# Performance work log

Hardware: AMD Instinct MI355X
Metric: run time of the kernel (lower is better)

## Reference

```python
import jax, jax.numpy as jnp
import numpy as np

B, C, S, H, W = 1, 256, 64, 32, 128
BLOCKS, HEADS, DH = 2, 8, 32
SCALE = DH ** (-0.5)


def layer_norm(x, w, b, eps=1e-5):
    mu = jnp.mean(x, axis=-1, keepdims=True)
    var = jnp.var(x, axis=-1, keepdims=True)
    return (x - mu) * jax.lax.rsqrt(var + eps) * w + b


def generate_y_for_attn(y, u):
    # y: (B,C,H,W), u: (B,S,S) float -> (B, S^2, 2H, C)
    Bv, Cv, Hv, Wv = y.shape
    Sv = u.shape[1]
    uf = jnp.floor(u).reshape(Bv, Sv * Sv)
    u_left = jnp.clip(uf, 0, Wv - 1).astype(jnp.int32)
    u_right = jnp.clip(uf + 1, 0, Wv - 1).astype(jnp.int32)
    yf = y.reshape(Bv, Cv * Hv, Wv)

    def gather_w(idx):
        idxb = jnp.broadcast_to(idx[:, None, :], (Bv, Cv * Hv, Sv * Sv))
        return jnp.take_along_axis(yf, idxb, axis=2).reshape(Bv, Cv, Hv, Sv * Sv)

    ys = jnp.concatenate([gather_w(u_left), gather_w(u_right)], axis=2)  # (B,C,2H,S2)
    return ys.transpose(0, 3, 2, 1)  # (B, S2, 2H, C)


def cross_attention(x, y, p, i):
    # x: (B,M,C), y: (B,M,N,C)
    q = layer_norm(x, p['ln_q_w'][i], p['ln_q_b'][i]) @ p['Wq'][i]        # (B,M,HD)
    k = layer_norm(y, p['ln_k_w'][i], p['ln_k_b'][i]) @ p['Wk'][i]        # (B,M,N,HD)
    v = layer_norm(y, p['ln_v_w'][i], p['ln_v_b'][i]) @ p['Wv'][i]        # (B,M,N,HD)
    Bv, M, _ = q.shape
    N = k.shape[2]
    q = q.reshape(Bv, M, HEADS, DH)
    k = k.reshape(Bv, M, N, HEADS, DH)
    v = v.reshape(Bv, M, N, HEADS, DH)
    dot = SCALE * jnp.einsum('bmhd,bmnhd->bhmn', q, k)                    # (B,H,M,N)
    attn = jax.nn.softmax(dot, axis=-1)
    a = jnp.einsum('bhmn,bmnhd->bmhd', attn, v).reshape(Bv, M, HEADS * DH)
    z = a @ p['Wproj'][i] + p['bproj'][i]
    z = layer_norm(z, p['ln_pre_w'][i], p['ln_pre_b'][i])
    h = jax.nn.gelu(z @ p['Wm1'][i] + p['bm1'][i], approximate=False)
    z = z + (h @ p['Wm2'][i] + p['bm2'][i])
    return layer_norm(z, p['ln_post_w'][i], p['ln_post_b'][i])


def setup_inputs() -> dict:
    key = jax.random.key(0)
    ks = jax.random.split(key, 16)
    std = 0.02
    inp = {
        'grd2sat': jax.random.normal(ks[0], (B, C, S, S), jnp.float32),
        'grd_x': jax.random.normal(ks[1], (B, C, H, W), jnp.float32),
        'u': jax.random.uniform(ks[2], (B, S, S), jnp.float32) * (W - 1),
        'ln_q_w': jnp.ones((BLOCKS, C)), 'ln_q_b': jnp.zeros((BLOCKS, C)),
        'ln_k_w': jnp.ones((BLOCKS, C)), 'ln_k_b': jnp.zeros((BLOCKS, C)),
        'ln_v_w': jnp.ones((BLOCKS, C)), 'ln_v_b': jnp.zeros((BLOCKS, C)),
        'Wq': std * jax.random.normal(ks[3], (BLOCKS, C, HEADS * DH)),
        'Wk': std * jax.random.normal(ks[4], (BLOCKS, C, HEADS * DH)),
        'Wv': std * jax.random.normal(ks[5], (BLOCKS, C, HEADS * DH)),
        'Wproj': std * jax.random.normal(ks[6], (BLOCKS, HEADS * DH, C)),
        'bproj': jnp.zeros((BLOCKS, C)),
        'ln_pre_w': jnp.ones((BLOCKS, C)), 'ln_pre_b': jnp.zeros((BLOCKS, C)),
        'Wm1': std * jax.random.normal(ks[7], (BLOCKS, C, 2 * C)),
        'bm1': jnp.zeros((BLOCKS, 2 * C)),
        'Wm2': std * jax.random.normal(ks[8], (BLOCKS, 2 * C, C)),
        'bm2': jnp.zeros((BLOCKS, C)),
        'ln_post_w': jnp.ones((BLOCKS, C)), 'ln_post_b': jnp.zeros((BLOCKS, C)),
    }
    return inp


def reference(grd2sat, grd_x, u, ln_q_w, ln_q_b, ln_k_w, ln_k_b, ln_v_w, ln_v_b,
              Wq, Wk, Wv, Wproj, bproj, ln_pre_w, ln_pre_b, Wm1, bm1, Wm2, bm2,
              ln_post_w, ln_post_b):
    p = dict(ln_q_w=ln_q_w, ln_q_b=ln_q_b, ln_k_w=ln_k_w, ln_k_b=ln_k_b,
             ln_v_w=ln_v_w, ln_v_b=ln_v_b, Wq=Wq, Wk=Wk, Wv=Wv, Wproj=Wproj,
             bproj=bproj, ln_pre_w=ln_pre_w, ln_pre_b=ln_pre_b, Wm1=Wm1, bm1=bm1,
             Wm2=Wm2, bm2=bm2, ln_post_w=ln_post_w, ln_post_b=ln_post_b)
    y_attn = generate_y_for_attn(grd_x, u)               # (B, S^2, 2H, C)
    x = grd2sat.reshape(B, C, S * S).transpose(0, 2, 1)  # (B, M, C)
    for i in range(BLOCKS):
        # (Swin self-attention layer omitted; cross-attention stack only.)
        x = cross_attention(x, y_attn, p, i)
    out = x.transpose(0, 2, 1).reshape(B, C, S, S)
    # L2 normalize over channel dim
    norm = jnp.sqrt(jnp.sum(out * out, axis=1, keepdims=True))
    return out / jnp.maximum(norm, 1e-12)
```

## Files before the change

### kernel.cpp

```cpp
#include <hip/hip_runtime.h>
#include <math.h>


#define C_DIM 256
#define M_DIM 4096
#define W_DIM 128
#define H_DIM 32
#define ATT_SCALE 0.17677669529663687f

typedef __attribute__((ext_vector_type(8))) short short8;
typedef __attribute__((ext_vector_type(4))) short short4v;
typedef __attribute__((ext_vector_type(4))) float floatx4;

__device__ __forceinline__ unsigned short f2bf(float f) {
    unsigned u = __float_as_uint(f);
    unsigned r = (u + 0x7fffu + ((u >> 16) & 1u)) >> 16;
    return (unsigned short)r;
}
__device__ __forceinline__ float gelu_exact(float x) {
    return 0.5f * x * (1.0f + erff(x * 0.70710678118654752f));
}

struct PrepArgs {
    const float* grd2sat; float* xcur;
// ... 92 lines not shown
        o.z = f2bf(tile[rq + 2][cl]);
        o.w = f2bf(tile[rq + 3][cl]);
        *(ushort4*)&out[(size_t)(c0 + cl) * R + r0 + rq] = o;
    } else if (b < 1418) {
        int jj = b - 1408;
        int N = a.fN[jj];
        int wcol = a.fwcol[jj] + t;
        const float* W = a.fW[jj];
        const float* lb = a.flnb[jj];
        float s = a.fbase[jj] ? a.fbase[jj][wcol] : 0.f;
        for (int k = 0; k < 256; ++k) s += lb[k] * W[(size_t)k * N + wcol];
        a.fout[jj][a.focol[jj] + t] = s;
    } else {
        int* hist = (int*)smemf;
        int* cur = (int*)smemf + 128;
        unsigned short* wlb = (unsigned short*)((int*)smemf + 256);
        if (t < 128) hist[t] = 0;
        __syncthreads();
        for (int it = 0; it < 16; ++it) {
            int m = it * 256 + t;
            int wl = (int)floorf(a.u[m]);
            wl = max(0, min(wl, 126));
            wlb[m] = (unsigned short)wl;
            atomicAdd(&hist[wl], 1);
        }
        __syncthreads();
        if (t == 0) {
            int run = 0, nc = 0;
            for (int bkt = 0; bkt < 127; ++bkt) {
                int c = hist[bkt];
                cur[bkt] = run;
                int q0 = run;
                while (c > 0) {
                    int take = min(c, 32);
                    a.chunks[nc] = make_int4(bkt, q0, take, 0);
                    ++nc; q0 += take; c -= take;
                }
                run += hist[bkt];
            }
            *a.nchunks = nc;
        }
        __syncthreads();
        for (int it = 0; it < 16; ++it) {
            int m = it * 256 + t;
            int wl = wlb[m];
            int pos = atomicAdd(&cur[wl], 1);
            a.perm[pos] = m;
        }
    }
}

struct GJ {
    const float* A; const unsigned short* Bt;
    const float* bias; const float* aw; const float* ab;
    const float* rw; const float* rb; const float* res;
    float* wrz; void* out; unsigned short* out2;
    int K, N;
};

template <int LN, int EPI, int OUTM, bool WRZ>
__device__ __forceinline__ void gemm_core(const GJ& j, short (*As)[264],
                                          short (*Bs)[264], int bm, int by) {
    int t = threadIdx.x;
    int bn = by << 6;
    int wv = t >> 6, lane = t & 63;
    int mt = wv & 1, nt0 = (wv >> 1) << 1;
    int quad = lane >> 4, l16 = lane & 15;
    floatx4 acc0 = {0.f, 0.f, 0.f, 0.f};
    floatx4 acc1 = {0.f, 0.f, 0.f, 0.f};
    const int K = j.K;
    for (int kc = 0; kc < K; kc += 256) {
        if (kc) __syncthreads();
        {
            int ar = t >> 3, cq = (t & 7) << 2;
            const float* ap = j.A + (size_t)(bm + ar) * K + kc + cq;
            float4 v[8];
#pragma unroll
            for (int g = 0; g < 8; ++g) v[g] = *(const float4*)(ap + g * 32);
            if (LN >= 1) {
                float s = 0.f, ss = 0.f;
#pragma unroll
                for (int g = 0; g < 8; ++g) {
                    s += v[g].x + v[g].y + v[g].z + v[g].w;
                    ss += v[g].x * v[g].x + v[g].y * v[g].y + v[g].z * v[g].z +
                          v[g].w * v[g].w;
                }
#pragma unroll
                for (int o = 1; o < 8; o <<= 1) {
                    s += __shfl_xor(s, o, 64);
                    ss += __shfl_xor(ss, o, 64);
                }
                float mu = s * (1.f / 256.f);
                float rs = rsqrtf(ss * (1.f / 256.f) - mu * mu + 1e-5f);
#pragma unroll
                for (int g = 0; g < 8; ++g) {
                    v[g].x = (v[g].x - mu) * rs;
                    v[g].y = (v[g].y - mu) * rs;
                    v[g].z = (v[g].z - mu) * rs;
                    v[g].w = (v[g].w - mu) * rs;
                }
                if (LN == 2) {
                    float s2 = 0.f, ss2 = 0.f;
#pragma unroll
                    for (int g = 0; g < 8; ++g) {
                        float4 w4 = *(const float4*)(j.aw + cq + g * 32);
                        float4 b4 = *(const float4*)(j.ab + cq + g * 32);
                        v[g].x = v[g].x * w4.x + b4.x;
                        v[g].y = v[g].y * w4.y + b4.y;
                        v[g].z = v[g].z * w4.z + b4.z;
                        v[g].w = v[g].w * w4.w + b4.w;
                        s2 += v[g].x + v[g].y + v[g].z + v[g].w;
                        ss2 += v[g].x * v[g].x + v[g].y * v[g].y +
                               v[g].z * v[g].z + v[g].w * v[g].w;
                    }
#pragma unroll
                    for (int o = 1; o < 8; o <<= 1) {
                        s2 += __shfl_xor(s2, o, 64);
                        ss2 += __shfl_xor(ss2, o, 64);
                    }
                    float mu2 = s2 * (1.f / 256.f);
                    float rs2 = rsqrtf(ss2 * (1.f / 256.f) - mu2 * mu2 + 1e-5f);
#pragma unroll
                    for (int g = 0; g < 8; ++g) {
                        v[g].x = (v[g].x - mu2) * rs2;
                        v[g].y = (v[g].y - mu2) * rs2;
                        v[g].z = (v[g].z - mu2) * rs2;
                        v[g].w = (v[g].w - mu2) * rs2;
                    }
                }
            }
            if (WRZ) {
                if (by == 0) {
#pragma unroll
                    for (int g = 0; g < 8; ++g)
                        *(float4*)&j.wrz[(size_t)(bm + ar) * 256 + cq + g * 32] =
                            v[g];
                }
            }
#pragma unroll
            for (int g = 0; g < 8; ++g) {
                short4v o;
                o[0] = (short)f2bf(v[g].x);
                o[1] = (short)f2bf(v[g].y);
                o[2] = (short)f2bf(v[g].z);
                o[3] = (short)f2bf(v[g].w);
                *(short4v*)&As[ar][cq + g * 32] = o;
            }
        }
        {
            int br = t >> 2, cq2 = (t & 3) << 3;
            const unsigned short* bp = j.Bt + (size_t)(bn + br) * K + kc + cq2;
#pragma unroll
            for (int g = 0; g < 8; ++g)
                *(short8*)&Bs[br][cq2 + g * 32] = *(const short8*)(bp + g * 32);
        }
        __syncthreads();
#pragma unroll
        for (int k0 = 0; k0 < 8; ++k0) {
            short8 aa = *(const short8*)&As[(mt << 4) + l16][(k0 << 5) + (quad << 3)];
            short8 b0 = *(const short8*)&Bs[(nt0 << 4) + l16][(k0 << 5) + (quad << 3)];
            short8 b1 =
                *(const short8*)&Bs[((nt0 + 1) << 4) + l16][(k0 << 5) + (quad << 3)];
            acc0 = __builtin_amdgcn_mfma_f32_16x16x32_bf16(aa, b0, acc0, 0, 0, 0);
            acc1 = __builtin_amdgcn_mfma_f32_16x16x32_bf16(aa, b1, acc1, 0, 0, 0);
        }
    }
#pragma unroll
    for (int jj = 0; jj < 2; ++jj) {
        const floatx4 accv = jj ? acc1 : acc0;
        int col = bn + ((nt0 + jj) << 4) + l16;
        float bv = j.bias ? j.bias[col] : 0.f;
#pragma unroll
        for (int r = 0; r < 4; ++r) {
            int row = bm + (mt << 4) + (quad << 2) + r;
            float v = accv[r] + bv;
            if (EPI == 1) v = gelu_exact(v);
            if (EPI == 2)
                v += j.res[(size_t)row * 256 + col] * j.rw[col] + j.rb[col];
            if (OUTM == 0) {
                ((float*)j.out)[(size_t)row * j.N + col] = v;
            } else if (OUTM == 1) {
                ((unsigned short*)j.out)[(size_t)row * 256 + col] = f2bf(v);
            } else {
                if (col < 256)
                    ((unsigned short*)j.out)[(size_t)row * 256 + col] = f2bf(v);
                else
                    j.out2[(size_t)(col - 256) * M_DIM + row] = f2bf(v);
            }
        }
    }
}

template <int MODE>
__global__ __launch_bounds__(256) void gemm_mode(GJ j0, GJ j1) {
    __shared__ short As[32][264];
    __shared__ short Bs[64][264];
    int bm = blockIdx.x << 5;
    if (MODE == 0) {
        if ((int)blockIdx.y < 4) gemm_core<1, 0, 1, false>(j0, As, Bs, bm, blockIdx.y);
        else gemm_core<0, 0, 2, false>(j1, As, Bs, bm, blockIdx.y - 4);
    } else if (MODE == 1) {
        if ((int)blockIdx.y < 4) gemm_core<2, 0, 1, false>(j0, As, Bs, bm, blockIdx.y);
        else gemm_core<0, 0, 2, false>(j1, As, Bs, bm, blockIdx.y - 4);
    } else if (MODE == 2) {
        gemm_core<0, 0, 0, false>(j0, As, Bs, bm, blockIdx.y);
    } else if (MODE == 3) {
        gemm_core<1, 1, 0, true>(j0, As, Bs, bm, blockIdx.y);
    } else {
        gemm_core<0, 2, 0, false>(j0, As, Bs, bm, blockIdx.y);
    }
}

__global__ __launch_bounds__(256) void attn_kernel(
    const unsigned short* __restrict__ Qb, const unsigned short* __restrict__ Kt,
    const unsigned short* __restrict__ Vt, const int* __restrict__ perm,
    const int4* __restrict__ chunks, const int* __restrict__ nchunks,
    float* __restrict__ Ao) {
    __shared__ short Qs[32][264];
    __shared__ short Ks[64][264];
    __shared__ short VsT[256][72];
    __shared__ float S[32][69];
    __shared__ short Pb[32][72];
    __shared__ int gperm[32];
    if ((int)blockIdx.x >= *nchunks) return;
    int4 cd = chunks[blockIdx.x];
    int wl = cd.x, qstart = cd.y, qcnt = cd.z;
    int t = threadIdx.x;
    if (t < 32) gperm[t] = (t < qcnt) ? perm[qstart + t] : 0;
    {
        int q = t >> 3, p = t & 7;
        if (q < qcnt) {
            const uint4* src =
                (const uint4*)(Qb + (size_t)perm[qstart + q] * 256 + (p << 5));
#pragma unroll
            for (int c = 0; c < 4; ++c) *(uint4*)&Qs[q][(p << 5) + (c << 3)] = src[c];
        } else {
            uint4 z = make_uint4(0, 0, 0, 0);
#pragma unroll
            for (int c = 0; c < 4; ++c) *(uint4*)&Qs[q][(p << 5) + (c << 3)] = z;
        }
    }
    {
        int n = t >> 2, p = t & 3;
        const uint4* src = (const uint4*)(Kt + ((size_t)(wl * 32 + n)) * 256 + (p << 6));
#pragma unroll
        for (int c = 0; c < 8; ++c) *(uint4*)&Ks[n][(p << 6) + (c << 3)] = src[c];
    }
    {
        const uint4* src = (const uint4*)(Vt + (size_t)t * M_DIM + (wl << 5));
#pragma unroll
        for (int c = 0; c < 8; ++c) *(uint4*)&VsT[t][c << 3] = src[c];
    }
    __syncthreads();
    int wv = t >> 6, lane = t & 63, quad = lane >> 4, l16 = lane & 15;
    int mtS = wv & 1, ntS0 = (wv >> 1) << 1;
    int mtP = wv & 1, ntP = wv >> 1;
    int sq = t >> 3, sg = t & 7;
#pragma unroll 1
    for (int h = 0; h < 8; ++h) {
        {
            short8 aa = *(const short8*)&Qs[(mtS << 4) + l16][(h << 5) + (quad << 3)];
            short8 b0 = *(const short8*)&Ks[(ntS0 << 4) + l16][(h << 5) + (quad << 3)];
            short8 b1 =
                *(const short8*)&Ks[((ntS0 + 1) << 4) + l16][(h << 5) + (quad << 3)];
            floatx4 z = {0.f, 0.f, 0.f, 0.f};
            floatx4 c0 = __builtin_amdgcn_mfma_f32_16x16x32_bf16(aa, b0, z, 0, 0, 0);
            floatx4 c1 = __builtin_amdgcn_mfma_f32_16x16x32_bf16(aa, b1, z, 0, 0, 0);
#pragma unroll
            for (int r = 0; r < 4; ++r) {
                int row = (mtS << 4) + (quad << 2) + r;
                S[row][(ntS0 << 4) + l16] = c0[r];
                S[row][((ntS0 + 1) << 4) + l16] = c1[r];
            }
        }
        __syncthreads();
        {
            float e[8];
            float s = 0.f;
#pragma unroll
            for (int c = 0; c < 8; ++c) {
                e[c] = __expf(S[sq][(sg << 3) + c] * ATT_SCALE);
                s += e[c];
            }
            s += __shfl_xor(s, 1, 64);
            s += __shfl_xor(s, 2, 64);
            s += __shfl_xor(s, 4, 64);
            float ri = 1.f / s;
#pragma unroll
            for (int c = 0; c < 8; ++c)
                Pb[sq][(sg << 3) + c] = (short)f2bf(e[c] * ri);
        }
        __syncthreads();
        {
            floatx4 acc = {0.f, 0.f, 0.f, 0.f};
#pragma unroll
            for (int ks = 0; ks < 2; ++ks) {
                short8 aa =
                    *(const short8*)&Pb[(mtP << 4) + l16][(ks << 5) + (quad << 3)];
                short8 bb = *(const short8*)&VsT[(h << 5) + (ntP << 4) + l16]
                                                [(ks << 5) + (quad << 3)];
                acc = __builtin_amdgcn_mfma_f32_16x16x32_bf16(aa, bb, acc, 0, 0, 0);
            }
#pragma unroll
            for (int r = 0; r < 4; ++r) {
                int q = (mtP << 4) + (quad << 2) + r;
                if (q < qcnt)
                    Ao[(size_t)gperm[q] * C_DIM + (h << 5) + (ntP << 4) + l16] =
                        acc[r];
            }
        }
        __syncthreads();
    }
}

__global__ __launch_bounds__(256) void out_kernel(const float* __restrict__ X,
                                                  const float* __restrict__ w,
                                                  const float* __restrict__ b,
                                                  float* __restrict__ out) {
    __shared__ float tile[64][65];
    int t = threadIdx.x;
    int mo = t >> 2, q = t & 3;
    int m0 = blockIdx.x << 6;
    const float* p = X + (size_t)(m0 + mo) * C_DIM + (q << 6);
    float4 v[16];
    float s = 0.f, ss = 0.f;
#pragma unroll
    for (int c = 0; c < 16; ++c) {
        v[c] = *(const float4*)(p + c * 4);
        s += v[c].x + v[c].y + v[c].z + v[c].w;
        ss += v[c].x * v[c].x + v[c].y * v[c].y + v[c].z * v[c].z + v[c].w * v[c].w;
    }
    s += __shfl_xor(s, 1, 64); s += __shfl_xor(s, 2, 64);
    ss += __shfl_xor(ss, 1, 64); ss += __shfl_xor(ss, 2, 64);
    float mu = s * (1.f / 256.f);
    float rs = rsqrtf(ss * (1.f / 256.f) - mu * mu + 1e-5f);
    float ss2 = 0.f;
#pragma unroll
    for (int c = 0; c < 16; ++c) {
        float4 w4 = *(const float4*)&w[(q << 6) + c * 4];
        float4 b4 = *(const float4*)&b[(q << 6) + c * 4];
        v[c].x = (v[c].x - mu) * rs * w4.x + b4.x;
        v[c].y = (v[c].y - mu) * rs * w4.y + b4.y;
        v[c].z = (v[c].z - mu) * rs * w4.z + b4.z;
        v[c].w = (v[c].w - mu) * rs * w4.w + b4.w;
// ... 20 lines not shown
        __syncthreads();
    }
}

extern "C" void kernel_launch(void* const* d_in, const int* in_sizes, int n_in,
                              void* d_out, int out_size, void* d_ws, size_t ws_size,
                              hipStream_t stream) {
    const float* grd2sat = (const float*)d_in[0];
    const float* grd_x   = (const float*)d_in[1];
    const float* u       = (const float*)d_in[2];
    const float* ln_q_w  = (const float*)d_in[3];
    const float* ln_q_b  = (const float*)d_in[4];
    const float* ln_k_w  = (const float*)d_in[5];
    const float* ln_k_b  = (const float*)d_in[6];
    const float* ln_v_w  = (const float*)d_in[7];
    const float* ln_v_b  = (const float*)d_in[8];
    const float* Wq      = (const float*)d_in[9];
    const float* Wk      = (const float*)d_in[10];
    const float* Wv      = (const float*)d_in[11];
    const float* Wproj   = (const float*)d_in[12];
    const float* bproj   = (const float*)d_in[13];
    const float* ln_pre_w = (const float*)d_in[14];
    const float* ln_pre_b = (const float*)d_in[15];
    const float* Wm1     = (const float*)d_in[16];
    const float* bm1     = (const float*)d_in[17];
    const float* Wm2     = (const float*)d_in[18];
    const float* bm2     = (const float*)d_in[19];
    const float* ln_post_w = (const float*)d_in[20];
    const float* ln_post_b = (const float*)d_in[21];

    float* ws   = (float*)d_ws;
    float* yhat = ws;
    float* xcur = ws + 1048576;
    float* zq   = ws + 2097152;
    float* abuf = ws + 3145728;
    float* hbuf = ws + 4194304;
    float* zbuf = ws + 6291456;
    unsigned short* Qb   = (unsigned short*)(ws + 7340032);
    unsigned short* Ktab = (unsigned short*)(ws + 7864320);
    unsigned short* Vt   = (unsigned short*)(ws + 8388608);
    unsigned short* Bt   = (unsigned short*)(ws + 8912896);
    float* biasbuf = ws + 9961472;
    int*  perm    = (int*)(ws + 9965568);
    int4* chunks  = (int4*)(ws + 9969664);
    int*  nchunks = (int*)(ws + 9970688);
    const size_t BS = 524288;
    const size_t OQ = 0, OKV = 65536, OP = 196608, OM1 = 262144, OM2 = 393216;

    dim3 b256(256);

    PrepArgs pa;
    pa.grd2sat = grd2sat; pa.xcur = xcur;
    pa.grd_x = grd_x;     pa.yhat = yhat;
    pa.u = u; pa.perm = perm; pa.chunks = chunks; pa.nchunks = nchunks;
    {
        int base = 0;
        for (int i = 0; i < 2; ++i) {
            int e = 6 * i;
            unsigned short* bt = Bt + i * BS;
            pa.win[e+0] = Wq + i * 65536;    pa.wout[e+0] = bt + OQ;
            pa.wlnw[e+0] = ln_q_w + i * 256; pa.wR[e+0] = 256; pa.wC[e+0] = 256;
            pa.win[e+1] = Wk + i * 65536;    pa.wout[e+1] = bt + OKV;
            pa.wlnw[e+1] = ln_k_w + i * 256; pa.wR[e+1] = 256; pa.wC[e+1] = 256;
            pa.win[e+2] = Wv + i * 65536;    pa.wout[e+2] = bt + OKV + 65536;
            pa.wlnw[e+2] = ln_v_w + i * 256; pa.wR[e+2] = 256; pa.wC[e+2] = 256;
            pa.win[e+3] = Wproj + i * 65536; pa.wout[e+3] = bt + OP;
            pa.wlnw[e+3] = nullptr;          pa.wR[e+3] = 256; pa.wC[e+3] = 256;
            pa.win[e+4] = Wm1 + i * 131072;  pa.wout[e+4] = bt + OM1;
            pa.wlnw[e+4] = ln_pre_w + i * 256; pa.wR[e+4] = 256; pa.wC[e+4] = 512;
            pa.win[e+5] = Wm2 + i * 131072;  pa.wout[e+5] = bt + OM2;
            pa.wlnw[e+5] = nullptr;          pa.wR[e+5] = 512; pa.wC[e+5] = 256;
        }
        for (int e = 0; e < 12; ++e) {
            pa.wbase[e] = base;
            base += (pa.wR[e] >> 5) * (pa.wC[e] >> 5);
        }
        pa.wbase[12] = base;
        for (int i = 0; i < 2; ++i) {
            int jb = 5 * i;
            float* bb = biasbuf + i * 1280;
            pa.fW[jb+0] = Wq + i * 65536; pa.flnb[jb+0] = ln_q_b + i * 256;
            pa.fbase[jb+0] = nullptr; pa.fout[jb+0] = bb;
            pa.fN[jb+0] = 256; pa.fwcol[jb+0] = 0; pa.focol[jb+0] = 0;
            pa.fW[jb+1] = Wk + i * 65536; pa.flnb[jb+1] = ln_k_b + i * 256;
            pa.fbase[jb+1] = nullptr; pa.fout[jb+1] = bb + 256;
            pa.fN[jb+1] = 256; pa.fwcol[jb+1] = 0; pa.focol[jb+1] = 0;
            pa.fW[jb+2] = Wv + i * 65536; pa.flnb[jb+2] = ln_v_b + i * 256;
            pa.fbase[jb+2] = nullptr; pa.fout[jb+2] = bb + 256;
            pa.fN[jb+2] = 256; pa.fwcol[jb+2] = 0; pa.focol[jb+2] = 256;
            pa.fW[jb+3] = Wm1 + i * 131072; pa.flnb[jb+3] = ln_pre_b + i * 256;
            pa.fbase[jb+3] = bm1 + i * 512; pa.fout[jb+3] = bb + 768;
            pa.fN[jb+3] = 512; pa.fwcol[jb+3] = 0; pa.focol[jb+3] = 0;
            pa.fW[jb+4] = Wm1 + i * 131072; pa.flnb[jb+4] = ln_pre_b + i * 256;
            pa.fbase[jb+4] = bm1 + i * 512; pa.fout[jb+4] = bb + 768;
            pa.fN[jb+4] = 512; pa.fwcol[jb+4] = 256; pa.focol[jb+4] = 256;
        }
    }
    prep_kernel<<<1419, b256, 0, stream>>>(pa);

    for (int i = 0; i < 2; ++i) {
        const unsigned short* bt = Bt + i * BS;
        float* bb = biasbuf + i * 1280;
        GJ jq = {};
        jq.A = xcur; jq.Bt = bt + OQ; jq.bias = bb;
        if (i == 1) { jq.aw = ln_post_w; jq.ab = ln_post_b; }
        jq.out = Qb; jq.K = 256; jq.N = 256;
        GJ jkv = {};
        jkv.A = yhat; jkv.Bt = bt + OKV; jkv.bias = bb + 256;
        jkv.out = Ktab; jkv.out2 = Vt; jkv.K = 256; jkv.N = 512;
        if (i == 0) gemm_mode<0><<<dim3(128, 12), b256, 0, stream>>>(jq, jkv);
        else        gemm_mode<1><<<dim3(128, 12), b256, 0, stream>>>(jq, jkv);

        attn_kernel<<<255, b256, 0, stream>>>(Qb, Ktab, Vt, perm, chunks,
                                              nchunks, abuf);

        GJ jp = {};
        jp.A = abuf; jp.Bt = bt + OP; jp.bias = bproj + i * 256;
        jp.out = zq; jp.K = 256; jp.N = 256;
        gemm_mode<2><<<dim3(128, 4), b256, 0, stream>>>(jp, jp);

        GJ jm1 = {};
        jm1.A = zq; jm1.Bt = bt + OM1; jm1.bias = bb + 768;
        jm1.out = hbuf; jm1.wrz = zbuf; jm1.K = 256; jm1.N = 512;
        gemm_mode<3><<<dim3(128, 8), b256, 0, stream>>>(jm1, jm1);

        GJ jm2 = {};
        jm2.A = hbuf; jm2.Bt = bt + OM2; jm2.bias = bm2 + i * 256;
        jm2.res = zbuf; jm2.rw = ln_pre_w + i * 256; jm2.rb = ln_pre_b + i * 256;
        jm2.out = xcur; jm2.K = 512; jm2.N = 256;
        gemm_mode<4><<<dim3(128, 4), b256, 0, stream>>>(jm2, jm2);
    }
    out_kernel<<<64, b256, 0, stream>>>(xcur, ln_post_w + 256, ln_post_b + 256,
                                        (float*)d_out);
}
```

Baseline: 220.8 us.

## Fuse Q-proj, attention, proj and MLP per block into one mega kernel

```diff
diff --git a/kernel.cpp b/kernel.cpp
--- a/kernel.cpp
+++ b/kernel.cpp
@@ -148,7 +148,7 @@
                 cur[bkt] = run;
                 int q0 = run;
                 while (c > 0) {
-                    int take = min(c, 32);
+                    int take = min(c, 16);
                     a.chunks[nc] = make_int4(bkt, q0, take, 0);
                     ++nc; q0 += take; c -= take;
                 }
@@ -166,266 +166,366 @@
     }
 }
 
-struct GJ {
-    const float* A; const unsigned short* Bt;
-    const float* bias; const float* aw; const float* ab;
-    const float* rw; const float* rb; const float* res;
-    float* wrz; void* out; unsigned short* out2;
-    int K, N;
+struct KVJob {
+    const float* A; const unsigned short* Bt; const float* bias;
+    unsigned short* Kt; unsigned short* Vt;
 };
 
-template <int LN, int EPI, int OUTM, bool WRZ>
-__device__ __forceinline__ void gemm_core(const GJ& j, short (*As)[264],
-                                          short (*Bs)[264], int bm, int by) {
+__global__ __launch_bounds__(256) void kv_gemm(KVJob j0, KVJob j1) {
+    __shared__ short As[32][264];
+    __shared__ short Bs[64][264];
+    const KVJob j = ((int)blockIdx.y < 8) ? j0 : j1;
+    int by = ((int)blockIdx.y < 8) ? blockIdx.y : blockIdx.y - 8;
     int t = threadIdx.x;
-    int bn = by << 6;
+    int bm = blockIdx.x << 5, bn = by << 6;
     int wv = t >> 6, lane = t & 63;
     int mt = wv & 1, nt0 = (wv >> 1) << 1;
     int quad = lane >> 4, l16 = lane & 15;
+    {
+        int ar = t >> 3, cq = (t & 7) << 2;
+        const float* ap = j.A + (size_t)(bm + ar) * 256 + cq;
+#pragma unroll
+        for (int g = 0; g < 8; ++g) {
+            float4 v = *(const float4*)(ap + g * 32);
+            short4v o;
+            o[0] = (short)f2bf(v.x);
+            o[1] = (short)f2bf(v.y);
+            o[2] = (short)f2bf(v.z);
+            o[3] = (short)f2bf(v.w);
+            *(short4v*)&As[ar][cq + g * 32] = o;
+        }
+    }
+    {
+        int br = t >> 2, o = (t & 3) << 6;
+        const unsigned short* bp = j.Bt + (size_t)(bn + br) * 256 + o;
+#pragma unroll
+        for (int c = 0; c < 8; ++c)
+            *(uint4*)&Bs[br][o + (c << 3)] = *(const uint4*)(bp + (c << 3));
+    }
+    __syncthreads();
     floatx4 acc0 = {0.f, 0.f, 0.f, 0.f};
     floatx4 acc1 = {0.f, 0.f, 0.f, 0.f};
-    const int K = j.K;
-    for (int kc = 0; kc < K; kc += 256) {
-        if (kc) __syncthreads();
-        {
-            int ar = t >> 3, cq = (t & 7) << 2;
-            const float* ap = j.A + (size_t)(bm + ar) * K + kc + cq;
-            float4 v[8];
-#pragma unroll
-            for (int g = 0; g < 8; ++g) v[g] = *(const float4*)(ap + g * 32);
-            if (LN >= 1) {
-                float s = 0.f, ss = 0.f;
-#pragma unroll
-                for (int g = 0; g < 8; ++g) {
-                    s += v[g].x + v[g].y + v[g].z + v[g].w;
-                    ss += v[g].x * v[g].x + v[g].y * v[g].y + v[g].z * v[g].z +
-                          v[g].w * v[g].w;
-                }
-#pragma unroll
-                for (int o = 1; o < 8; o <<= 1) {
-                    s += __shfl_xor(s, o, 64);
-                    ss += __shfl_xor(ss, o, 64);
-                }
-                float mu = s * (1.f / 256.f);
-                float rs = rsqrtf(ss * (1.f / 256.f) - mu * mu + 1e-5f);
-#pragma unroll
-                for (int g = 0; g < 8; ++g) {
-                    v[g].x = (v[g].x - mu) * rs;
-                    v[g].y = (v[g].y - mu) * rs;
-                    v[g].z = (v[g].z - mu) * rs;
-                    v[g].w = (v[g].w - mu) * rs;
-                }
-                if (LN == 2) {
-                    float s2 = 0.f, ss2 = 0.f;
-#pragma unroll
-                    for (int g = 0; g < 8; ++g) {
-                        float4 w4 = *(const float4*)(j.aw + cq + g * 32);
-                        float4 b4 = *(const float4*)(j.ab + cq + g * 32);
-                        v[g].x = v[g].x * w4.x + b4.x;
-                        v[g].y = v[g].y * w4.y + b4.y;
-                        v[g].z = v[g].z * w4.z + b4.z;
-                        v[g].w = v[g].w * w4.w + b4.w;
-                        s2 += v[g].x + v[g].y + v[g].z + v[g].w;
-                        ss2 += v[g].x * v[g].x + v[g].y * v[g].y +
-                               v[g].z * v[g].z + v[g].w * v[g].w;
-                    }
-#pragma unroll
-                    for (int o = 1; o < 8; o <<= 1) {
-                        s2 += __shfl_xor(s2, o, 64);
-                        ss2 += __shfl_xor(ss2, o, 64);
-                    }
-                    float mu2 = s2 * (1.f / 256.f);
-                    float rs2 = rsqrtf(ss2 * (1.f / 256.f) - mu2 * mu2 + 1e-5f);
-#pragma unroll
-                    for (int g = 0; g < 8; ++g) {
-                        v[g].x = (v[g].x - mu2) * rs2;
-                        v[g].y = (v[g].y - mu2) * rs2;
-                        v[g].z = (v[g].z - mu2) * rs2;
-                        v[g].w = (v[g].w - mu2) * rs2;
-                    }
-                }
-            }
-            if (WRZ) {
-                if (by == 0) {
-#pragma unroll
-                    for (int g = 0; g < 8; ++g)
-                        *(float4*)&j.wrz[(size_t)(bm + ar) * 256 + cq + g * 32] =
-                            v[g];
-                }
-            }
-#pragma unroll
-            for (int g = 0; g < 8; ++g) {
-                short4v o;
-                o[0] = (short)f2bf(v[g].x);
-                o[1] = (short)f2bf(v[g].y);
-                o[2] = (short)f2bf(v[g].z);
-                o[3] = (short)f2bf(v[g].w);
-                *(short4v*)&As[ar][cq + g * 32] = o;
-            }
-        }
-        {
-            int br = t >> 2, cq2 = (t & 3) << 3;
-            const unsigned short* bp = j.Bt + (size_t)(bn + br) * K + kc + cq2;
-#pragma unroll
-            for (int g = 0; g < 8; ++g)
-                *(short8*)&Bs[br][cq2 + g * 32] = *(const short8*)(bp + g * 32);
-        }
-        __syncthreads();
-#pragma unroll
-        for (int k0 = 0; k0 < 8; ++k0) {
-            short8 aa = *(const short8*)&As[(mt << 4) + l16][(k0 << 5) + (quad << 3)];
-            short8 b0 = *(const short8*)&Bs[(nt0 << 4) + l16][(k0 << 5) + (quad << 3)];
-            short8 b1 =
-                *(const short8*)&Bs[((nt0 + 1) << 4) + l16][(k0 << 5) + (quad << 3)];
-            acc0 = __builtin_amdgcn_mfma_f32_16x16x32_bf16(aa, b0, acc0, 0, 0, 0);
-            acc1 = __builtin_amdgcn_mfma_f32_16x16x32_bf16(aa, b1, acc1, 0, 0, 0);
-        }
+#pragma unroll
+    for (int k0 = 0; k0 < 8; ++k0) {
+        short8 aa = *(const short8*)&As[(mt << 4) + l16][(k0 << 5) + (quad << 3)];
+        short8 b0 = *(const short8*)&Bs[(nt0 << 4) + l16][(k0 << 5) + (quad << 3)];
+        short8 b1 =
+            *(const short8*)&Bs[((nt0 + 1) << 4) + l16][(k0 << 5) + (quad << 3)];
+        acc0 = __builtin_amdgcn_mfma_f32_16x16x32_bf16(aa, b0, acc0, 0, 0, 0);
+        acc1 = __builtin_amdgcn_mfma_f32_16x16x32_bf16(aa, b1, acc1, 0, 0, 0);
     }
 #pragma unroll
     for (int jj = 0; jj < 2; ++jj) {
         const floatx4 accv = jj ? acc1 : acc0;
         int col = bn + ((nt0 + jj) << 4) + l16;
-        float bv = j.bias ? j.bias[col] : 0.f;
+        float bv = j.bias[col];
 #pragma unroll
         for (int r = 0; r < 4; ++r) {
             int row = bm + (mt << 4) + (quad << 2) + r;
             float v = accv[r] + bv;
-            if (EPI == 1) v = gelu_exact(v);
-            if (EPI == 2)
-                v += j.res[(size_t)row * 256 + col] * j.rw[col] + j.rb[col];
-            if (OUTM == 0) {
-                ((float*)j.out)[(size_t)row * j.N + col] = v;
-            } else if (OUTM == 1) {
-                ((unsigned short*)j.out)[(size_t)row * 256 + col] = f2bf(v);
-            } else {
-                if (col < 256)
-                    ((unsigned short*)j.out)[(size_t)row * 256 + col] = f2bf(v);
-                else
-                    j.out2[(size_t)(col - 256) * M_DIM + row] = f2bf(v);
-            }
+            if (col < 256)
+                j.Kt[(size_t)row * 256 + col] = f2bf(v);
+            else
+                j.Vt[(size_t)(col - 256) * M_DIM + row] = f2bf(v);
         }
     }
 }
 
-template <int MODE>
-__global__ __launch_bounds__(256) void gemm_mode(GJ j0, GJ j1) {
-    __shared__ short As[32][264];
+template <int LNM>
+__global__ __launch_bounds__(256) void mega_kernel(
+    const float* __restrict__ xin, float* __restrict__ xout,
+    const unsigned short* __restrict__ Kt, const unsigned short* __restrict__ Vtab,
+    const unsigned short* __restrict__ Wq, const unsigned short* __restrict__ Wp,
+    const unsigned short* __restrict__ Wm1, const unsigned short* __restrict__ Wm2,
+    const float* __restrict__ bq, const float* __restrict__ bp,
+    const float* __restrict__ bm1f, const float* __restrict__ bm2,
+    const float* __restrict__ rw, const float* __restrict__ rb,
+    const float* __restrict__ aw, const float* __restrict__ ab,
+    const int* __restrict__ perm, const int4* __restrict__ chunks,
+    const int* __restrict__ nchunks) {
     __shared__ short Bs[64][264];
-    int bm = blockIdx.x << 5;
-    if (MODE == 0) {
-        if ((int)blockIdx.y < 4) gemm_core<1, 0, 1, false>(j0, As, Bs, bm, blockIdx.y);
-        else gemm_core<0, 0, 2, false>(j1, As, Bs, bm, blockIdx.y - 4);
-    } else if (MODE == 1) {
-        if ((int)blockIdx.y < 4) gemm_core<2, 0, 1, false>(j0, As, Bs, bm, blockIdx.y);
-        else gemm_core<0, 0, 2, false>(j1, As, Bs, bm, blockIdx.y - 4);
-    } else if (MODE == 2) {
-        gemm_core<0, 0, 0, false>(j0, As, Bs, bm, blockIdx.y);
-    } else if (MODE == 3) {
-        gemm_core<1, 1, 0, true>(j0, As, Bs, bm, blockIdx.y);
-    } else {
-        gemm_core<0, 2, 0, false>(j0, As, Bs, bm, blockIdx.y);
-    }
-}
-
-__global__ __launch_bounds__(256) void attn_kernel(
-    const unsigned short* __restrict__ Qb, const unsigned short* __restrict__ Kt,
-    const unsigned short* __restrict__ Vt, const int* __restrict__ perm,
-    const int4* __restrict__ chunks, const int* __restrict__ nchunks,
-    float* __restrict__ Ao) {
-    __shared__ short Qs[32][264];
-    __shared__ short Ks[64][264];
     __shared__ short VsT[256][72];
-    __shared__ float S[32][69];
-    __shared__ short Pb[32][72];
-    __shared__ int gperm[32];
+    __shared__ short Xs[16][264];
+    __shared__ short Qs[16][264];
+    __shared__ short Os[16][264];
+    __shared__ float Zs[16][260];
+    __shared__ short Hs[16][528];
+    __shared__ float Ss[16][68];
+    __shared__ short Pb[16][72];
+    __shared__ int gq[16];
     if ((int)blockIdx.x >= *nchunks) return;
     int4 cd = chunks[blockIdx.x];
-    int wl = cd.x, qstart = cd.y, qcnt = cd.z;
+    int wl = cd.x, q0 = cd.y, qcnt = cd.z;
     int t = threadIdx.x;
-    if (t < 32) gperm[t] = (t < qcnt) ? perm[qstart + t] : 0;
+    int wv = t >> 6, lane = t & 63, quad = lane >> 4, l16 = lane & 15;
+    if (t < 16) gq[t] = perm[q0 + min(t, qcnt - 1)];
+    __syncthreads();
     {
-        int q = t >> 3, p = t & 7;
-        if (q < qcnt) {
-            const uint4* src =
-                (const uint4*)(Qb + (size_t)perm[qstart + q] * 256 + (p << 5));
-#pragma unroll
-            for (int c = 0; c < 4; ++c) *(uint4*)&Qs[q][(p << 5) + (c << 3)] = src[c];
-        } else {
-            uint4 z = make_uint4(0, 0, 0, 0);
-#pragma unroll
-            for (int c = 0; c < 4; ++c) *(uint4*)&Qs[q][(p << 5) + (c << 3)] = z;
-        }
+        int row = t >> 4, seg = t & 15;
+        const float* xp = xin + (size_t)gq[row] * 256 + (seg << 4);
+        float4 v[4];
+#pragma unroll
+        for (int c = 0; c < 4; ++c) v[c] = *(const float4*)(xp + (c << 2));
+        float s = 0.f, ss = 0.f;
+#pragma unroll
+        for (int c = 0; c < 4; ++c) {
+            s += v[c].x + v[c].y + v[c].z + v[c].w;
+            ss += v[c].x * v[c].x + v[c].y * v[c].y + v[c].z * v[c].z +
+                  v[c].w * v[c].w;
+        }
+#pragma unroll
+        for (int o = 1; o < 16; o <<= 1) {
+            s += __shfl_xor(s, o, 64);
+            ss += __shfl_xor(ss, o, 64);
+        }
+        float mu = s * (1.f / 256.f);
+        float rs = rsqrtf(ss * (1.f / 256.f) - mu * mu + 1e-5f);
+#pragma unroll
+        for (int c = 0; c < 4; ++c) {
+            v[c].x = (v[c].x - mu) * rs;
+            v[c].y = (v[c].y - mu) * rs;
+            v[c].z = (v[c].z - mu) * rs;
+            v[c].w = (v[c].w - mu) * rs;
+        }
+        if (LNM == 2) {
+            float s2 = 0.f, ss2 = 0.f;
+#pragma unroll
+            for (int c = 0; c < 4; ++c) {
+                float4 w4 = *(const float4*)&aw[(seg << 4) + (c << 2)];
+                float4 b4 = *(const float4*)&ab[(seg << 4) + (c << 2)];
+                v[c].x = v[c].x * w4.x + b4.x;
+                v[c].y = v[c].y * w4.y + b4.y;
+                v[c].z = v[c].z * w4.z + b4.z;
+                v[c].w = v[c].w * w4.w + b4.w;
+                s2 += v[c].x + v[c].y + v[c].z + v[c].w;
+                ss2 += v[c].x * v[c].x + v[c].y * v[c].y + v[c].z * v[c].z +
+                       v[c].w * v[c].w;
+            }
+#pragma unroll
+            for (int o = 1; o < 16; o <<= 1) {
+                s2 += __shfl_xor(s2, o, 64);
+                ss2 += __shfl_xor(ss2, o, 64);
+            }
+            float mu2 = s2 * (1.f / 256.f);
+            float rs2 = rsqrtf(ss2 * (1.f / 256.f) - mu2 * mu2 + 1e-5f);
+#pragma unroll
+            for (int c = 0; c < 4; ++c) {
+                v[c].x = (v[c].x - mu2) * rs2;
+                v[c].y = (v[c].y - mu2) * rs2;
+                v[c].z = (v[c].z - mu2) * rs2;
+                v[c].w = (v[c].w - mu2) * rs2;
+            }
+        }
+#pragma unroll
+        for (int c = 0; c < 4; ++c) {
+            short4v o;
+            o[0] = (short)f2bf(v[c].x);
+            o[1] = (short)f2bf(v[c].y);
+            o[2] = (short)f2bf(v[c].z);
+            o[3] = (short)f2bf(v[c].w);
+            *(short4v*)&Xs[row][(seg << 4) + (c << 2)] = o;
+        }
+    }
+    __syncthreads();
+#pragma unroll 1
+    for (int nc = 0; nc < 4; ++nc) {
+        {
+            int br = t >> 2, o = (t & 3) << 6;
+            const unsigned short* bp2 = Wq + (size_t)((nc << 6) + br) * 256 + o;
+#pragma unroll
+            for (int c = 0; c < 8; ++c)
+                *(uint4*)&Bs[br][o + (c << 3)] = *(const uint4*)(bp2 + (c << 3));
+        }
+        __syncthreads();
+        floatx4 acc = {0.f, 0.f, 0.f, 0.f};
+#pragma unroll
+        for (int k0 = 0; k0 < 8; ++k0) {
+            short8 aa = *(const short8*)&Xs[l16][(k0 << 5) + (quad << 3)];
+            short8 bb2 = *(const short8*)&Bs[(wv << 4) + l16][(k0 << 5) + (quad << 3)];
+            acc = __builtin_amdgcn_mfma_f32_16x16x32_bf16(aa, bb2, acc, 0, 0, 0);
+        }
+        int nb = (nc << 6) + (wv << 4);
+        float bv = bq[nb + l16];
+#pragma unroll
+        for (int r = 0; r < 4; ++r)
+            Qs[(quad << 2) + r][nb + l16] = (short)f2bf(acc[r] + bv);
+        __syncthreads();
     }
     {
-        int n = t >> 2, p = t & 3;
-        const uint4* src = (const uint4*)(Kt + ((size_t)(wl * 32 + n)) * 256 + (p << 6));
-#pragma unroll
-        for (int c = 0; c < 8; ++c) *(uint4*)&Ks[n][(p << 6) + (c << 3)] = src[c];
-    }
-    {
-        const uint4* src = (const uint4*)(Vt + (size_t)t * M_DIM + (wl << 5));
-#pragma unroll
-        for (int c = 0; c < 8; ++c) *(uint4*)&VsT[t][c << 3] = src[c];
+        int br = t >> 2, o = (t & 3) << 6;
+        const unsigned short* kp = Kt + ((size_t)(wl << 5) + br) * 256 + o;
+#pragma unroll
+        for (int c = 0; c < 8; ++c)
+            *(uint4*)&Bs[br][o + (c << 3)] = *(const uint4*)(kp + (c << 3));
+        const unsigned short* vp = Vtab + (size_t)t * M_DIM + (wl << 5);
+#pragma unroll
+        for (int c = 0; c < 8; ++c)
+            *(uint4*)&VsT[t][c << 3] = *(const uint4*)(vp + (c << 3));
     }
     __syncthreads();
-    int wv = t >> 6, lane = t & 63, quad = lane >> 4, l16 = lane & 15;
-    int mtS = wv & 1, ntS0 = (wv >> 1) << 1;
-    int mtP = wv & 1, ntP = wv >> 1;
-    int sq = t >> 3, sg = t & 7;
 #pragma unroll 1
     for (int h = 0; h < 8; ++h) {
         {
-            short8 aa = *(const short8*)&Qs[(mtS << 4) + l16][(h << 5) + (quad << 3)];
-            short8 b0 = *(const short8*)&Ks[(ntS0 << 4) + l16][(h << 5) + (quad << 3)];
-            short8 b1 =
-                *(const short8*)&Ks[((ntS0 + 1) << 4) + l16][(h << 5) + (quad << 3)];
+            short8 aa = *(const short8*)&Qs[l16][(h << 5) + (quad << 3)];
+            short8 bb2 = *(const short8*)&Bs[(wv << 4) + l16][(h << 5) + (quad << 3)];
             floatx4 z = {0.f, 0.f, 0.f, 0.f};
-            floatx4 c0 = __builtin_amdgcn_mfma_f32_16x16x32_bf16(aa, b0, z, 0, 0, 0);
-            floatx4 c1 = __builtin_amdgcn_mfma_f32_16x16x32_bf16(aa, b1, z, 0, 0, 0);
-#pragma unroll
-            for (int r = 0; r < 4; ++r) {
-                int row = (mtS << 4) + (quad << 2) + r;
-                S[row][(ntS0 << 4) + l16] = c0[r];
-                S[row][((ntS0 + 1) << 4) + l16] = c1[r];
-            }
+            floatx4 c0 = __builtin_amdgcn_mfma_f32_16x16x32_bf16(aa, bb2, z, 0, 0, 0);
+#pragma unroll
+            for (int r = 0; r < 4; ++r)
+                Ss[(quad << 2) + r][(wv << 4) + l16] = c0[r];
         }
         __syncthreads();
         {
-            float e[8];
+            int row = t >> 4, seg = t & 15;
+            float e[4];
             float s = 0.f;
 #pragma unroll
-            for (int c = 0; c < 8; ++c) {
-                e[c] = __expf(S[sq][(sg << 3) + c] * ATT_SCALE);
+            for (int c = 0; c < 4; ++c) {
+                e[c] = __expf(Ss[row][(seg << 2) + c] * ATT_SCALE);
                 s += e[c];
             }
-            s += __shfl_xor(s, 1, 64);
-            s += __shfl_xor(s, 2, 64);
-            s += __shfl_xor(s, 4, 64);
+#pragma unroll
+            for (int o = 1; o < 16; o <<= 1) s += __shfl_xor(s, o, 64);
             float ri = 1.f / s;
 #pragma unroll
+            for (int c = 0; c < 4; ++c)
+                Pb[row][(seg << 2) + c] = (short)f2bf(e[c] * ri);
+        }
+        __syncthreads();
+        if (wv < 2) {
+            floatx4 acc = {0.f, 0.f, 0.f, 0.f};
+#pragma unroll
+            for (int ks = 0; ks < 2; ++ks) {
+                short8 aa = *(const short8*)&Pb[l16][(ks << 5) + (quad << 3)];
+                short8 bb2 = *(const short8*)&VsT[(h << 5) + (wv << 4) + l16]
+                                                 [(ks << 5) + (quad << 3)];
+                acc = __builtin_amdgcn_mfma_f32_16x16x32_bf16(aa, bb2, acc, 0, 0, 0);
+            }
+#pragma unroll
+            for (int r = 0; r < 4; ++r)
+                Os[(quad << 2) + r][(h << 5) + (wv << 4) + l16] =
+                    (short)f2bf(acc[r]);
+        }
+        __syncthreads();
+    }
+#pragma unroll 1
+    for (int nc = 0; nc < 4; ++nc) {
+        {
+            int br = t >> 2, o = (t & 3) << 6;
+            const unsigned short* bp2 = Wp + (size_t)((nc << 6) + br) * 256 + o;
+#pragma unroll
             for (int c = 0; c < 8; ++c)
-                Pb[sq][(sg << 3) + c] = (short)f2bf(e[c] * ri);
-        }
-        __syncthreads();
+                *(uint4*)&Bs[br][o + (c << 3)] = *(const uint4*)(bp2 + (c << 3));
+        }
+        __syncthreads();
+        floatx4 acc = {0.f, 0.f, 0.f, 0.f};
+#pragma unroll
+        for (int k0 = 0; k0 < 8; ++k0) {
+            short8 aa = *(const short8*)&Os[l16][(k0 << 5) + (quad << 3)];
+            short8 bb2 = *(const short8*)&Bs[(wv << 4) + l16][(k0 << 5) + (quad << 3)];
+            acc = __builtin_amdgcn_mfma_f32_16x16x32_bf16(aa, bb2, acc, 0, 0, 0);
+        }
+        int nb = (nc << 6) + (wv << 4);
+        float bv = bp[nb + l16];
+#pragma unroll
+        for (int r = 0; r < 4; ++r)
+            Zs[(quad << 2) + r][nb + l16] = acc[r] + bv;
+        __syncthreads();
+    }
+    {
+        int row = t >> 4, seg = t & 15;
+        float4 v[4];
+#pragma unroll
+        for (int c = 0; c < 4; ++c)
+            v[c] = *(const float4*)&Zs[row][(seg << 4) + (c << 2)];
+        float s = 0.f, ss = 0.f;
+#pragma unroll
+        for (int c = 0; c < 4; ++c) {
+            s += v[c].x + v[c].y + v[c].z + v[c].w;
+            ss += v[c].x * v[c].x + v[c].y * v[c].y + v[c].z * v[c].z +
+                  v[c].w * v[c].w;
+        }
+#pragma unroll
+        for (int o = 1; o < 16; o <<= 1) {
+            s += __shfl_xor(s, o, 64);
+            ss += __shfl_xor(ss, o, 64);
+        }
+        float mu = s * (1.f / 256.f);
+        float rs = rsqrtf(ss * (1.f / 256.f) - mu * mu + 1e-5f);
+#pragma unroll
+        for (int c = 0; c < 4; ++c) {
+            v[c].x = (v[c].x - mu) * rs;
+            v[c].y = (v[c].y - mu) * rs;
+            v[c].z = (v[c].z - mu) * rs;
+            v[c].w = (v[c].w - mu) * rs;
+            *(float4*)&Zs[row][(seg << 4) + (c << 2)] = v[c];
+            short4v o;
+            o[0] = (short)f2bf(v[c].x);
+            o[1] = (short)f2bf(v[c].y);
+            o[2] = (short)f2bf(v[c].z);
+            o[3] = (short)f2bf(v[c].w);
+            *(short4v*)&Xs[row][(seg << 4) + (c << 2)] = o;
+        }
+    }
+    __syncthreads();
+#pragma unroll 1
+    for (int nc = 0; nc < 8; ++nc) {
         {
-            floatx4 acc = {0.f, 0.f, 0.f, 0.f};
-#pragma unroll
-            for (int ks = 0; ks < 2; ++ks) {
+            int br = t >> 2, o = (t & 3) << 6;
+            const unsigned short* bp2 = Wm1 + (size_t)((nc << 6) + br) * 256 + o;
+#pragma unroll
+            for (int c = 0; c < 8; ++c)
+                *(uint4*)&Bs[br][o + (c << 3)] = *(const uint4*)(bp2 + (c << 3));
+        }
+        __syncthreads();
+        floatx4 acc = {0.f, 0.f, 0.f, 0.f};
+#pragma unroll
+        for (int k0 = 0; k0 < 8; ++k0) {
+            short8 aa = *(const short8*)&Xs[l16][(k0 << 5) + (quad << 3)];
+            short8 bb2 = *(const short8*)&Bs[(wv << 4) + l16][(k0 << 5) + (quad << 3)];
+            acc = __builtin_amdgcn_mfma_f32_16x16x32_bf16(aa, bb2, acc, 0, 0, 0);
+        }
+        int nb = (nc << 6) + (wv << 4);
+        float bv = bm1f[nb + l16];
+#pragma unroll
+        for (int r = 0; r < 4; ++r)
+            Hs[(quad << 2) + r][nb + l16] = (short)f2bf(gelu_exact(acc[r] + bv));
+        __syncthreads();
+    }
+#pragma unroll 1
+    for (int nc = 0; nc < 4; ++nc) {
+        floatx4 acc = {0.f, 0.f, 0.f, 0.f};
+#pragma unroll 1
+        for (int kh = 0; kh < 2; ++kh) {
+            {
+                int br = t >> 2, o = (t & 3) << 6;
+                const unsigned short* bp2 =
+                    Wm2 + (size_t)((nc << 6) + br) * 512 + (kh << 8) + o;
+#pragma unroll
+                for (int c = 0; c < 8; ++c)
+                    *(uint4*)&Bs[br][o + (c << 3)] = *(const uint4*)(bp2 + (c << 3));
+            }
+            __syncthreads();
+#pragma unroll
+            for (int k0 = 0; k0 < 8; ++k0) {
                 short8 aa =
-                    *(const short8*)&Pb[(mtP << 4) + l16][(ks << 5) + (quad << 3)];
-                short8 bb = *(const short8*)&VsT[(h << 5) + (ntP << 4) + l16]
-                                                [(ks << 5) + (quad << 3)];
-                acc = __builtin_amdgcn_mfma_f32_16x16x32_bf16(aa, bb, acc, 0, 0, 0);
-            }
-#pragma unroll
-            for (int r = 0; r < 4; ++r) {
-                int q = (mtP << 4) + (quad << 2) + r;
-                if (q < qcnt)
-                    Ao[(size_t)gperm[q] * C_DIM + (h << 5) + (ntP << 4) + l16] =
-                        acc[r];
-            }
-        }
-        __syncthreads();
+                    *(const short8*)&Hs[l16][(kh << 8) + (k0 << 5) + (quad << 3)];
+                short8 bb2 =
+                    *(const short8*)&Bs[(wv << 4) + l16][(k0 << 5) + (quad << 3)];
+                acc = __builtin_amdgcn_mfma_f32_16x16x32_bf16(aa, bb2, acc, 0, 0, 0);
+            }
+            __syncthreads();
+        }
+        int nb = (nc << 6) + (wv << 4);
+        int col = nb + l16;
+        float bv = bm2[col], rwv = rw[col], rbv = rb[col];
+#pragma unroll
+        for (int r = 0; r < 4; ++r) {
+            int row = (quad << 2) + r;
+            if (row < qcnt)
+                xout[(size_t)gq[row] * 256 + col] =
+                    acc[r] + bv + Zs[row][col] * rwv + rbv;
+        }
     }
 }
 
@@ -512,18 +612,17 @@
     float* ws   = (float*)d_ws;
     float* yhat = ws;
     float* xcur = ws + 1048576;
-    float* zq   = ws + 2097152;
-    float* abuf = ws + 3145728;
-    float* hbuf = ws + 4194304;
-    float* zbuf = ws + 6291456;
-    unsigned short* Qb   = (unsigned short*)(ws + 7340032);
-    unsigned short* Ktab = (unsigned short*)(ws + 7864320);
-    unsigned short* Vt   = (unsigned short*)(ws + 8388608);
-    unsigned short* Bt   = (unsigned short*)(ws + 8912896);
-    float* biasbuf = ws + 9961472;
-    int*  perm    = (int*)(ws + 9965568);
-    int4* chunks  = (int4*)(ws + 9969664);
-    int*  nchunks = (int*)(ws + 9970688);
+    float* xb1  = ws + 2097152;
+    float* xb2  = ws + 3145728;
+    unsigned short* Ktab0 = (unsigned short*)(ws + 4194304);
+    unsigned short* Vt0   = (unsigned short*)(ws + 4718592);
+    unsigned short* Ktab1 = (unsigned short*)(ws + 5242880);
+    unsigned short* Vt1   = (unsigned short*)(ws + 5767168);
+    unsigned short* Bt    = (unsigned short*)(ws + 6291456);
+    float* biasbuf = ws + 6815744;
+    int*  perm    = (int*)(ws + 6818304);
+    int4* chunks  = (int4*)(ws + 6822400);
+    int*  nchunks = (int*)(ws + 6824448);
     const size_t BS = 524288;
     const size_t OQ = 0, OKV = 65536, OP = 196608, OM1 = 262144, OM2 = 393216;
 
@@ -578,38 +677,20 @@
     }
     prep_kernel<<<1419, b256, 0, stream>>>(pa);
 
-    for (int i = 0; i < 2; ++i) {
-        const unsigned short* bt = Bt + i * BS;
-        float* bb = biasbuf + i * 1280;
-        GJ jq = {};
-        jq.A = xcur; jq.Bt = bt + OQ; jq.bias = bb;
-        if (i == 1) { jq.aw = ln_post_w; jq.ab = ln_post_b; }
-        jq.out = Qb; jq.K = 256; jq.N = 256;
-        GJ jkv = {};
-        jkv.A = yhat; jkv.Bt = bt + OKV; jkv.bias = bb + 256;
-        jkv.out = Ktab; jkv.out2 = Vt; jkv.K = 256; jkv.N = 512;
-        if (i == 0) gemm_mode<0><<<dim3(128, 12), b256, 0, stream>>>(jq, jkv);
-        else        gemm_mode<1><<<dim3(128, 12), b256, 0, stream>>>(jq, jkv);
-
-        attn_kernel<<<255, b256, 0, stream>>>(Qb, Ktab, Vt, perm, chunks,
-                                              nchunks, abuf);
-
-        GJ jp = {};
-        jp.A = abuf; jp.Bt = bt + OP; jp.bias = bproj + i * 256;
-        jp.out = zq; jp.K = 256; jp.N = 256;
-        gemm_mode<2><<<dim3(128, 4), b256, 0, stream>>>(jp, jp);
-
-        GJ jm1 = {};
-        jm1.A = zq; jm1.Bt = bt + OM1; jm1.bias = bb + 768;
-        jm1.out = hbuf; jm1.wrz = zbuf; jm1.K = 256; jm1.N = 512;
-        gemm_mode<3><<<dim3(128, 8), b256, 0, stream>>>(jm1, jm1);
-
-        GJ jm2 = {};
-        jm2.A = hbuf; jm2.Bt = bt + OM2; jm2.bias = bm2 + i * 256;
-        jm2.res = zbuf; jm2.rw = ln_pre_w + i * 256; jm2.rb = ln_pre_b + i * 256;
-        jm2.out = xcur; jm2.K = 512; jm2.N = 256;
-        gemm_mode<4><<<dim3(128, 4), b256, 0, stream>>>(jm2, jm2);
-    }
-    out_kernel<<<64, b256, 0, stream>>>(xcur, ln_post_w + 256, ln_post_b + 256,
+    KVJob k0 = {yhat, Bt + OKV, biasbuf + 256, Ktab0, Vt0};
+    KVJob k1 = {yhat, Bt + BS + OKV, biasbuf + 1280 + 256, Ktab1, Vt1};
+    kv_gemm<<<dim3(128, 16), b256, 0, stream>>>(k0, k1);
+
+    mega_kernel<1><<<384, b256, 0, stream>>>(
+        xcur, xb1, Ktab0, Vt0, Bt + OQ, Bt + OP, Bt + OM1, Bt + OM2,
+        biasbuf, bproj, biasbuf + 768, bm2, ln_pre_w, ln_pre_b,
+        nullptr, nullptr, perm, chunks, nchunks);
+    mega_kernel<2><<<384, b256, 0, stream>>>(
+        xb1, xb2, Ktab1, Vt1, Bt + BS + OQ, Bt + BS + OP, Bt + BS + OM1,
+        Bt + BS + OM2, biasbuf + 1280, bproj + 256, biasbuf + 1280 + 768,
+        bm2 + 256, ln_pre_w + 256, ln_pre_b + 256, ln_post_w, ln_post_b,
+        perm, chunks, nchunks);
+
+    out_kernel<<<64, b256, 0, stream>>>(xb2, ln_post_w + 256, ln_post_b + 256,
                                         (float*)d_out);
 }
```

Result: slower. 346.1 us (+56.8%).

## Fuse output projection GEMM into attention kernel via shared-memory tile

Applied to the files above, without the earlier changes.

```diff
diff --git a/kernel.cpp b/kernel.cpp
--- a/kernel.cpp
+++ b/kernel.cpp
@@ -318,8 +318,6 @@
     } else if (MODE == 1) {
         if ((int)blockIdx.y < 4) gemm_core<2, 0, 1, false>(j0, As, Bs, bm, blockIdx.y);
         else gemm_core<0, 0, 2, false>(j1, As, Bs, bm, blockIdx.y - 4);
-    } else if (MODE == 2) {
-        gemm_core<0, 0, 0, false>(j0, As, Bs, bm, blockIdx.y);
     } else if (MODE == 3) {
         gemm_core<1, 1, 0, true>(j0, As, Bs, bm, blockIdx.y);
     } else {
@@ -327,14 +325,16 @@
     }
 }
 
-__global__ __launch_bounds__(256) void attn_kernel(
+__global__ __launch_bounds__(256) void attn_proj_kernel(
     const unsigned short* __restrict__ Qb, const unsigned short* __restrict__ Kt,
-    const unsigned short* __restrict__ Vt, const int* __restrict__ perm,
+    const unsigned short* __restrict__ Vt, const unsigned short* __restrict__ Wp,
+    const float* __restrict__ bp, const int* __restrict__ perm,
     const int4* __restrict__ chunks, const int* __restrict__ nchunks,
-    float* __restrict__ Ao) {
+    float* __restrict__ Zo) {
     __shared__ short Qs[32][264];
     __shared__ short Ks[64][264];
     __shared__ short VsT[256][72];
+    __shared__ short Os[32][264];
     __shared__ float S[32][69];
     __shared__ short Pb[32][72];
     __shared__ int gperm[32];
@@ -365,28 +365,28 @@
     {
         const uint4* src = (const uint4*)(Vt + (size_t)t * M_DIM + (wl << 5));
 #pragma unroll
-        for (int c = 0; c < 8; ++c) *(uint4*)&VsT[t][c << 3] = src[c];
+        for (int c = 0; c < 8; ++c) *(uint4*)&VsT[t][c << 3] = *(const uint4*)&src[c];
     }
     __syncthreads();
     int wv = t >> 6, lane = t & 63, quad = lane >> 4, l16 = lane & 15;
-    int mtS = wv & 1, ntS0 = (wv >> 1) << 1;
-    int mtP = wv & 1, ntP = wv >> 1;
+    int mt = wv & 1, nt0 = (wv >> 1) << 1;
+    int ntP = wv >> 1;
     int sq = t >> 3, sg = t & 7;
 #pragma unroll 1
     for (int h = 0; h < 8; ++h) {
         {
-            short8 aa = *(const short8*)&Qs[(mtS << 4) + l16][(h << 5) + (quad << 3)];
-            short8 b0 = *(const short8*)&Ks[(ntS0 << 4) + l16][(h << 5) + (quad << 3)];
+            short8 aa = *(const short8*)&Qs[(mt << 4) + l16][(h << 5) + (quad << 3)];
+            short8 b0 = *(const short8*)&Ks[(nt0 << 4) + l16][(h << 5) + (quad << 3)];
             short8 b1 =
-                *(const short8*)&Ks[((ntS0 + 1) << 4) + l16][(h << 5) + (quad << 3)];
+                *(const short8*)&Ks[((nt0 + 1) << 4) + l16][(h << 5) + (quad << 3)];
             floatx4 z = {0.f, 0.f, 0.f, 0.f};
             floatx4 c0 = __builtin_amdgcn_mfma_f32_16x16x32_bf16(aa, b0, z, 0, 0, 0);
             floatx4 c1 = __builtin_amdgcn_mfma_f32_16x16x32_bf16(aa, b1, z, 0, 0, 0);
 #pragma unroll
             for (int r = 0; r < 4; ++r) {
-                int row = (mtS << 4) + (quad << 2) + r;
-                S[row][(ntS0 << 4) + l16] = c0[r];
-                S[row][((ntS0 + 1) << 4) + l16] = c1[r];
+                int row = (mt << 4) + (quad << 2) + r;
+                S[row][(nt0 << 4) + l16] = c0[r];
+                S[row][((nt0 + 1) << 4) + l16] = c1[r];
             }
         }
         __syncthreads();
@@ -412,17 +412,49 @@
 #pragma unroll
             for (int ks = 0; ks < 2; ++ks) {
                 short8 aa =
-                    *(const short8*)&Pb[(mtP << 4) + l16][(ks << 5) + (quad << 3)];
+                    *(const short8*)&Pb[(mt << 4) + l16][(ks << 5) + (quad << 3)];
                 short8 bb = *(const short8*)&VsT[(h << 5) + (ntP << 4) + l16]
                                                 [(ks << 5) + (quad << 3)];
                 acc = __builtin_amdgcn_mfma_f32_16x16x32_bf16(aa, bb, acc, 0, 0, 0);
             }
 #pragma unroll
+            for (int r = 0; r < 4; ++r)
+                Os[(mt << 4) + (quad << 2) + r][(h << 5) + (ntP << 4) + l16] =
+                    (short)f2bf(acc[r]);
+        }
+        __syncthreads();
+    }
+#pragma unroll 1
+    for (int nc = 0; nc < 4; ++nc) {
+        {
+            int br = t >> 2, o = (t & 3) << 6;
+            const unsigned short* wp2 = Wp + (size_t)((nc << 6) + br) * 256 + o;
+#pragma unroll
+            for (int c = 0; c < 8; ++c)
+                *(uint4*)&Ks[br][o + (c << 3)] = *(const uint4*)(wp2 + (c << 3));
+        }
+        __syncthreads();
+        floatx4 acc0 = {0.f, 0.f, 0.f, 0.f};
+        floatx4 acc1 = {0.f, 0.f, 0.f, 0.f};
+#pragma unroll
+        for (int k0 = 0; k0 < 8; ++k0) {
+            short8 aa = *(const short8*)&Os[(mt << 4) + l16][(k0 << 5) + (quad << 3)];
+            short8 b0 = *(const short8*)&Ks[(nt0 << 4) + l16][(k0 << 5) + (quad << 3)];
+            short8 b1 =
+                *(const short8*)&Ks[((nt0 + 1) << 4) + l16][(k0 << 5) + (quad << 3)];
+            acc0 = __builtin_amdgcn_mfma_f32_16x16x32_bf16(aa, b0, acc0, 0, 0, 0);
+            acc1 = __builtin_amdgcn_mfma_f32_16x16x32_bf16(aa, b1, acc1, 0, 0, 0);
+        }
+#pragma unroll
+        for (int jj = 0; jj < 2; ++jj) {
+            const floatx4 av = jj ? acc1 : acc0;
+            int col = (nc << 6) + ((nt0 + jj) << 4) + l16;
+            float bv = bp[col];
+#pragma unroll
             for (int r = 0; r < 4; ++r) {
-                int q = (mtP << 4) + (quad << 2) + r;
+                int q = (mt << 4) + (quad << 2) + r;
                 if (q < qcnt)
-                    Ao[(size_t)gperm[q] * C_DIM + (h << 5) + (ntP << 4) + l16] =
-                        acc[r];
+                    Zo[(size_t)gperm[q] * C_DIM + col] = av[r] + bv;
             }
         }
         __syncthreads();
@@ -513,7 +545,6 @@
     float* yhat = ws;
     float* xcur = ws + 1048576;
     float* zq   = ws + 2097152;
-    float* abuf = ws + 3145728;
     float* hbuf = ws + 4194304;
     float* zbuf = ws + 6291456;
     unsigned short* Qb   = (unsigned short*)(ws + 7340032);
@@ -591,13 +622,8 @@
         if (i == 0) gemm_mode<0><<<dim3(128, 12), b256, 0, stream>>>(jq, jkv);
         else        gemm_mode<1><<<dim3(128, 12), b256, 0, stream>>>(jq, jkv);
 
-        attn_kernel<<<255, b256, 0, stream>>>(Qb, Ktab, Vt, perm, chunks,
-                                              nchunks, abuf);
-
-        GJ jp = {};
-        jp.A = abuf; jp.Bt = bt + OP; jp.bias = bproj + i * 256;
-        jp.out = zq; jp.K = 256; jp.N = 256;
-        gemm_mode<2><<<dim3(128, 4), b256, 0, stream>>>(jp, jp);
+        attn_proj_kernel<<<320, b256, 0, stream>>>(
+            Qb, Ktab, Vt, bt + OP, bproj + i * 256, perm, chunks, nchunks, zq);
 
         GJ jm1 = {};
         jm1.A = zq; jm1.Bt = bt + OM1; jm1.bias = bb + 768;
```

Measured after the change: 232.0 us. 1.05x slower.
